# Kernel tuning notes

Hardware: AMD Instinct MI355X
Metric: run time of the kernel (lower is better)

The kernel has to match this reference:

```python
import jax, jax.numpy as jnp
import numpy as np

B, S, D = 4, 8192, 1024
NC = 5
EPS = 1e-5  # nn.LayerNorm default eps


def setup_inputs() -> dict:
    key = jax.random.key(0)
    kx, kid, kg, kb, ks, kw, kbias = jax.random.split(key, 7)
    x = jax.random.normal(kx, (B, S, D), dtype=jnp.float32)
    compartment_ids = jax.random.randint(kid, (B, S), 0, NC)
    # per-compartment LayerNorm affine params (stacked) and scaling
    gamma = 1.0 + 0.1 * jax.random.normal(kg, (NC, D), dtype=jnp.float32)
    beta = 0.1 * jax.random.normal(kb, (NC, D), dtype=jnp.float32)
    scale = 1.0 + 0.1 * jax.random.normal(ks, (NC,), dtype=jnp.float32)
    # compartment_transition_norm: nn.Linear(d_model, d_model)
    W = jax.random.normal(kw, (D, D), dtype=jnp.float32) / np.sqrt(D)
    b = 0.01 * jax.random.normal(kbias, (D,), dtype=jnp.float32)
    return {"x": x, "compartment_ids": compartment_ids, "gamma": gamma,
            "beta": beta, "scale": scale, "W": W, "b": b}


def reference(x, compartment_ids, gamma, beta, scale, W, b):
    # tokens with id >= NC are left untouched (original guard)
    valid = compartment_ids < NC                      # [B,S]
    cid = jnp.clip(compartment_ids, 0, NC - 1)        # safe gather index
    # per-token LayerNorm statistics over last dim (biased variance)
    mu = jnp.mean(x, axis=-1, keepdims=True)
    var = jnp.mean(jnp.square(x - mu), axis=-1, keepdims=True)
    normed = (x - mu) * jax.lax.rsqrt(var + EPS)      # [B,S,D]
    g = gamma[cid]                                    # [B,S,D]
    bt = beta[cid]                                    # [B,S,D]
    s = scale[cid][..., None]                         # [B,S,1]
    y = (normed * g + bt) * s
    y = jnp.where(valid[..., None], y, x)
    # residual transition: x + Linear(x)
    return y + jnp.einsum('bsd,ed->bse', y, W) + b
```

## Files before the change

kernel.cpp:

```cpp
#include <hip/hip_runtime.h>
#include <stdint.h>

#define NCOMP 5
#define DM 1024
#define LN_EPS 1e-5f

typedef __attribute__((ext_vector_type(8))) __bf16 bf16x8;
typedef __attribute__((ext_vector_type(4))) float f32x4;

__device__ __forceinline__ unsigned short f2bf(float f) {
    unsigned u = __builtin_bit_cast(unsigned, f);
    u += 0x7fffu + ((u >> 16) & 1u);
    return (unsigned short)(u >> 16);
}

__global__ __launch_bounds__(256) void ln_w_kernel(
    const float* __restrict__ x, const int* __restrict__ cid,
    const float* __restrict__ gamma, const float* __restrict__ beta,
    const float* __restrict__ scale, const float* __restrict__ W,
    unsigned short* __restrict__ y, unsigned short* __restrict__ Wb, int M)
{
    const int lane = threadIdx.x & 63;
    const int t = blockIdx.x * 4 + (threadIdx.x >> 6);

    if (t < M) {
        const float* xp = x + (size_t)t * DM;
        float4 v[4];
#pragma unroll
        for (int q = 0; q < 4; ++q)
            v[q] = *(const float4*)(xp + q * 256 + lane * 4);

        float s = 0.f, ss = 0.f;
#pragma unroll
        for (int q = 0; q < 4; ++q) {
            s  += v[q].x + v[q].y + v[q].z + v[q].w;
            ss += v[q].x*v[q].x + v[q].y*v[q].y + v[q].z*v[q].z + v[q].w*v[q].w;
        }
#pragma unroll
        for (int off = 32; off; off >>= 1) {
            s  += __shfl_xor(s, off);
            ss += __shfl_xor(ss, off);
        }
        const float mu  = s * (1.0f / DM);
        const float var = ss * (1.0f / DM) - mu * mu;
        const float rs  = rsqrtf(var + LN_EPS);

        const int craw  = cid[t];
        const bool valid = craw < NCOMP;
        const int c = min(max(craw, 0), NCOMP - 1);
        const float sc = scale[c];
        const float* gp = gamma + (size_t)c * DM;
        const float* bp = beta  + (size_t)c * DM;
        unsigned short* yp = y + (size_t)t * DM;
#pragma unroll
        for (int q = 0; q < 4; ++q) {
            const int e = q * 256 + lane * 4;
            const float4 g  = *(const float4*)(gp + e);
            const float4 bb = *(const float4*)(bp + e);
            const float o0 = valid ? ((v[q].x - mu) * rs * g.x + bb.x) * sc : v[q].x;
            const float o1 = valid ? ((v[q].y - mu) * rs * g.y + bb.y) * sc : v[q].y;
            const float o2 = valid ? ((v[q].z - mu) * rs * g.z + bb.z) * sc : v[q].z;
            const float o3 = valid ? ((v[q].w - mu) * rs * g.w + bb.w) * sc : v[q].w;
            uint2 p;
            p.x = (unsigned)f2bf(o0) | ((unsigned)f2bf(o1) << 16);
            p.y = (unsigned)f2bf(o2) | ((unsigned)f2bf(o3) << 16);
            *(uint2*)(yp + e) = p;
        }
    } else if (t < M + DM) {
        const int row = t - M;
        const float* wp = W + (size_t)row * DM;
        unsigned short* wo = Wb + (size_t)row * DM;
#pragma unroll
        for (int q = 0; q < 4; ++q) {
            const int e = q * 256 + lane * 4;
            float4 a = *(const float4*)(wp + e);
            a.x += (e + 0 == row) ? 1.0f : 0.0f;
            a.y += (e + 1 == row) ? 1.0f : 0.0f;
            a.z += (e + 2 == row) ? 1.0f : 0.0f;
            a.w += (e + 3 == row) ? 1.0f : 0.0f;
            uint2 p;
            p.x = (unsigned)f2bf(a.x) | ((unsigned)f2bf(a.y) << 16);
            p.y = (unsigned)f2bf(a.z) | ((unsigned)f2bf(a.w) << 16);
            *(uint2*)(wo + e) = p;
        }
    }
}

__device__ __forceinline__ void gld16(const unsigned short* g, unsigned short* l) {
    __builtin_amdgcn_global_load_lds(
        (const __attribute__((address_space(1))) unsigned int*)(uintptr_t)g,
        (__attribute__((address_space(3))) unsigned int*)(uintptr_t)l,
        16, 0, 0);
}

#define GEMM_ITER(T, CA, CAB, CB, NA, NAB, NB)                                \
  {                                                                           \
    const int t_ = (T);                                                       \
                \
    __builtin_amdgcn_s_setprio(1);                                            \
    _Pragma("unroll")                                                         \
    for (int j = 0; j < 4; ++j)                                               \
        _Pragma("unroll")                                                     \
        for (int n = 0; n < 4; ++n)                                           \
            acc[j][n] = __builtin_amdgcn_mfma_f32_16x16x32_bf16(              \
                CB[n], CA[j], acc[j][n], 0, 0, 0);                            \
    __builtin_amdgcn_s_setprio(0);                                            \
                                 \
    if (t_ < 29) {                                                            \
        unsigned short* stg = smem + ((t_ + 3) & 3) * BUF;                    \
        const int kn = (t_ + 3) * 32;                                         \
        gld16(gA0 + kn, stg + sA0);                                           \
        gld16(gA1 + kn, stg + sA1);                                           \
        gld16(gB0 + kn, stg + sB0);                                           \
        gld16(gB1 + kn, stg + sB1);                                           \
    }                                                                         \
       \
    if (t_ < 29)       { asm volatile("s_waitcnt vmcnt(8)" ::: "memory"); }   \
    else if (t_ == 29) { asm volatile("s_waitcnt vmcnt(4)" ::: "memory"); }   \
    else               { asm volatile("s_waitcnt vmcnt(0)" ::: "memory"); }   \
    __builtin_amdgcn_s_barrier();         \
                \
    if (t_ < 31) {                                                            \
        const unsigned short* An = smem + ((t_ + 1) & 3) * BUF;               \
        const unsigned short* Bn = An + 8192;                                 \
        _Pragma("unroll")                                                     \
        for (int j = 0; j < 4; ++j)                                           \
            NB[j] = *(const bf16x8*)&Bn[(wn + j * 16) * 32 + loff];           \
        _Pragma("unroll")                                                     \
        for (int j = 0; j < 4; ++j)                                           \
            NA[j] = *(const bf16x8*)&An[(wm + j * 16) * 32 + loff];           \
    }                                                                         \
              \
    __builtin_amdgcn_s_setprio(1);                                            \
    _Pragma("unroll")                                                         \
    for (int j = 0; j < 4; ++j)                                               \
        _Pragma("unroll")                                                     \
        for (int n = 0; n < 4; ++n)                                           \
            acc[4 + j][n] = __builtin_amdgcn_mfma_f32_16x16x32_bf16(          \
                CB[n], CAB[j], acc[4 + j][n], 0, 0, 0);                       \
    __builtin_amdgcn_s_setprio(0);                                            \
             \
    if (t_ < 31) {                                                            \
        const unsigned short* An = smem + ((t_ + 1) & 3) * BUF;               \
        _Pragma("unroll")                                                     \
        for (int j = 0; j < 4; ++j)                                           \
            NAB[j] = *(const bf16x8*)&An[(wm + 64 + j * 16) * 32 + loff];     \
    }                                                                         \
  }

__global__ __launch_bounds__(512, 2) void gemm_kernel(
    const unsigned short* __restrict__ A,
    const unsigned short* __restrict__ Bp,
    const float* __restrict__ bias,
    float* __restrict__ C, int M)
{
    constexpr int K = 1024, N = 1024;
    constexpr int BUF = 16384;
    __shared__ __align__(16) unsigned short smem[4 * BUF];

    const int tid  = threadIdx.x;
    const int lane = tid & 63;
    const int wave = tid >> 6;
    const int wm   = (wave >> 2) * 128;
    const int wn   = (wave & 3) * 64;

    const int nwg = gridDim.x;
    int wg = blockIdx.x;
    if ((nwg & 7) == 0) wg = (wg & 7) * (nwg >> 3) + (wg >> 3);
    const int bm = (wg >> 2) * 256;
    const int bn = (wg & 3) * 256;

    const int qsrc = (((lane & 3) ^ ((lane >> 3) & 3))) * 8;
    const int rA0  = (wave * 2) * 16 + (lane >> 2);
    const unsigned short* gA0 = A  + (size_t)(bm + rA0) * K + qsrc;
    const unsigned short* gA1 = A  + (size_t)(bm + rA0 + 16) * K + qsrc;
    const unsigned short* gB0 = Bp + (size_t)(bn + rA0) * K + qsrc;
    const unsigned short* gB1 = Bp + (size_t)(bn + rA0 + 16) * K + qsrc;
    const int sA0 = (wave * 2) * 512 + lane * 8;
    const int sA1 = sA0 + 512;
    const int sB0 = 8192 + sA0;
    const int sB1 = 8192 + sA1;

    const int fr   = lane & 15;
    const int quad = lane >> 4;
    const int loff = fr * 32 + ((quad ^ ((fr >> 1) & 3)) * 8);

    f32x4 acc[8][4] = {};

#pragma unroll
    for (int kt = 0; kt < 3; ++kt) {
        unsigned short* sb = smem + kt * BUF;
        gld16(gA0 + kt * 32, sb + sA0);
        gld16(gA1 + kt * 32, sb + sA1);
        gld16(gB0 + kt * 32, sb + sB0);
        gld16(gB1 + kt * 32, sb + sB1);
    }
    asm volatile("s_waitcnt vmcnt(8)" ::: "memory");
    __builtin_amdgcn_s_barrier();

    bf16x8 afA0[4], afB0[4], bfr0[4], afA1[4], afB1[4], bfr1[4];
    {
        const unsigned short* A0 = smem;
        const unsigned short* B0 = smem + 8192;
#pragma unroll
        for (int j = 0; j < 4; ++j)
            bfr0[j] = *(const bf16x8*)&B0[(wn + j * 16) * 32 + loff];
#pragma unroll
        for (int j = 0; j < 4; ++j)
            afA0[j] = *(const bf16x8*)&A0[(wm + j * 16) * 32 + loff];
#pragma unroll
        for (int j = 0; j < 4; ++j)
            afB0[j] = *(const bf16x8*)&A0[(wm + 64 + j * 16) * 32 + loff];
    }

    for (int t = 0; t < 32; t += 2) {
        GEMM_ITER(t,     afA0, afB0, bfr0, afA1, afB1, bfr1)
        GEMM_ITER(t + 1, afA1, afB1, bfr1, afA0, afB0, bfr0)
    }

    float* tb = (float*)smem + wave * 1088;
    const int q4 = quad * 4;
    const float4 bvT = *(const float4*)&bias[bn + wn + fr * 4];
#pragma unroll
    for (int mi = 0; mi < 8; ++mi) {
#pragma unroll
        for (int ni = 0; ni < 4; ++ni)
            *(float4*)&tb[fr * 68 + ni * 16 + q4] = *(const float4*)&acc[mi][ni];
#pragma unroll
        for (int j = 0; j < 4; ++j) {
            const int row = j * 4 + quad;
            const float4 v = *(const float4*)&tb[row * 68 + fr * 4];
            float4 o;
            o.x = v.x + bvT.x; o.y = v.y + bvT.y;
            o.z = v.z + bvT.z; o.w = v.w + bvT.w;
            *(float4*)&C[(size_t)(bm + wm + mi * 16 + row) * N + bn + wn + fr * 4] = o;
        }
    }
}

extern "C" void kernel_launch(void* const* d_in, const int* in_sizes, int n_in,
                              void* d_out, int out_size, void* d_ws, size_t ws_size,
                              hipStream_t stream)
{
    const float* x     = (const float*)d_in[0];
    const int*   cid   = (const int*)d_in[1];
    const float* gamma = (const float*)d_in[2];
    const float* beta  = (const float*)d_in[3];
    const float* scale = (const float*)d_in[4];
    const float* W     = (const float*)d_in[5];
    const float* bias  = (const float*)d_in[6];
    float* out = (float*)d_out;

    const int M = in_sizes[0] / DM;
    unsigned short* yb = (unsigned short*)d_ws;
    unsigned short* Wb = yb + (size_t)M * DM;

    ln_w_kernel<<<(M + DM) / 4, 256, 0, stream>>>(x, cid, gamma, beta, scale, W, yb, Wb, M);
    gemm_kernel<<<dim3((M / 256) * 4), 512, 0, stream>>>(yb, Wb, bias, out, M);
}
```

Measured before the change: 307.4 us.

## Process two output tiles per GEMM workgroup with cross-tile prefetch

Each GEMM workgroup now computes two 256x256 output tiles in sequence and halves the grid. During the first tile's final k-steps it prefetches the second tile's first stages, so the pipeline does not drain between tiles. The epilogue moves to a swizzled staging buffer in the fourth LDS stage so it does not overwrite prefetched data. This amortises prologue/epilogue latency, but leaves fewer workgroups and may hurt load balance or occupancy.

```diff
diff --git a/kernel.cpp b/kernel.cpp
--- a/kernel.cpp
+++ b/kernel.cpp
@@ -93,7 +93,7 @@
         16, 0, 0);
 }
 
-#define GEMM_ITER(T, CA, CAB, CB, NA, NAB, NB)                                \
+#define GEMM_ITER(T, MODE, CA, CAB, CB, NA, NAB, NB)                          \
   {                                                                           \
     const int t_ = (T);                                                       \
                 \
@@ -105,7 +105,7 @@
             acc[j][n] = __builtin_amdgcn_mfma_f32_16x16x32_bf16(              \
                 CB[n], CA[j], acc[j][n], 0, 0, 0);                            \
     __builtin_amdgcn_s_setprio(0);                                            \
-                                 \
+     \
     if (t_ < 29) {                                                            \
         unsigned short* stg = smem + ((t_ + 3) & 3) * BUF;                    \
         const int kn = (t_ + 3) * 32;                                         \
@@ -113,14 +113,23 @@
         gld16(gA1 + kn, stg + sA1);                                           \
         gld16(gB0 + kn, stg + sB0);                                           \
         gld16(gB1 + kn, stg + sB1);                                           \
-    }                                                                         \
-       \
-    if (t_ < 29)       { asm volatile("s_waitcnt vmcnt(8)" ::: "memory"); }   \
-    else if (t_ == 29) { asm volatile("s_waitcnt vmcnt(4)" ::: "memory"); }   \
-    else               { asm volatile("s_waitcnt vmcnt(0)" ::: "memory"); }   \
+    } else if (MODE == 0) {                                                   \
+               \
+        unsigned short* stg = smem + ((t_ + 3) & 3) * BUF;                    \
+        const int kn2 = (t_ - 29) * 32;                                       \
+        gld16(gA0 + kn2 + dA, stg + sA0);                                     \
+        gld16(gA1 + kn2 + dA, stg + sA1);                                     \
+        gld16(gB0 + kn2 + dB, stg + sB0);                                     \
+        gld16(gB1 + kn2 + dB, stg + sB1);                                     \
+    }                                                                         \
+           \
+    if (MODE == 0 || t_ < 29) { asm volatile("s_waitcnt vmcnt(8)" ::: "memory"); } \
+    else if (t_ == 29)        { asm volatile("s_waitcnt vmcnt(4)" ::: "memory"); } \
+    else                      { asm volatile("s_waitcnt vmcnt(0)" ::: "memory"); } \
     __builtin_amdgcn_s_barrier();         \
-                \
-    if (t_ < 31) {                                                            \
+          \
+          \
+    if (MODE == 0 || t_ < 31) {                                               \
         const unsigned short* An = smem + ((t_ + 1) & 3) * BUF;               \
         const unsigned short* Bn = An + 8192;                                 \
         _Pragma("unroll")                                                     \
@@ -140,11 +149,35 @@
                 CB[n], CAB[j], acc[4 + j][n], 0, 0, 0);                       \
     __builtin_amdgcn_s_setprio(0);                                            \
              \
-    if (t_ < 31) {                                                            \
+    if (MODE == 0 || t_ < 31) {                                               \
         const unsigned short* An = smem + ((t_ + 1) & 3) * BUF;               \
         _Pragma("unroll")                                                     \
         for (int j = 0; j < 4; ++j)                                           \
             NAB[j] = *(const bf16x8*)&An[(wm + 64 + j * 16) * 32 + loff];     \
+    }                                                                         \
+  }
+
+#define EPILOGUE()                                                            \
+  {                                                                           \
+    float* tb = (float*)(smem + 3 * BUF) + wave * 1024;                       \
+    const float4 bvT = *(const float4*)&bias[bn + wn + fr * 4];               \
+    _Pragma("unroll")                                                         \
+    for (int mi = 0; mi < 8; ++mi) {                                          \
+        _Pragma("unroll")                                                     \
+        for (int ni = 0; ni < 4; ++ni)                                        \
+            *(float4*)&tb[fr * 64 + (((ni * 4 + quad) ^ ((fr & 7) << 1)) * 4)]\
+                = *(const float4*)&acc[mi][ni];                               \
+        _Pragma("unroll")                                                     \
+        for (int j = 0; j < 4; ++j) {                                         \
+            const int row = j * 4 + quad;                                     \
+            const float4 v = *(const float4*)                                 \
+                &tb[row * 64 + ((fr ^ ((row & 7) << 1)) * 4)];                \
+            float4 o;                                                         \
+            o.x = v.x + bvT.x; o.y = v.y + bvT.y;                             \
+            o.z = v.z + bvT.z; o.w = v.w + bvT.w;                             \
+            *(float4*)&C[(size_t)(bm + wm + mi * 16 + row) * N                \
+                         + bn + wn + fr * 4] = o;                             \
+        }                                                                     \
     }                                                                         \
   }
 
@@ -164,11 +197,17 @@
     const int wm   = (wave >> 2) * 128;
     const int wn   = (wave & 3) * 64;
 
-    const int nwg = gridDim.x;
-    int wg = blockIdx.x;
-    if ((nwg & 7) == 0) wg = (wg & 7) * (nwg >> 3) + (wg >> 3);
-    const int bm = (wg >> 2) * 256;
-    const int bn = (wg & 3) * 256;
+    const int nwg = gridDim.x * 2;
+    const int wge0 = blockIdx.x;
+    const int wge1 = blockIdx.x + gridDim.x;
+    const int wg0 = (wge0 & 7) * (nwg >> 3) + (wge0 >> 3);
+    const int wg1 = (wge1 & 7) * (nwg >> 3) + (wge1 >> 3);
+    const int bm0 = (wg0 >> 2) * 256, bn0 = (wg0 & 3) * 256;
+    const int bm1 = (wg1 >> 2) * 256, bn1 = (wg1 & 3) * 256;
+    const ptrdiff_t dA = (ptrdiff_t)(bm1 - bm0) * K;
+    const ptrdiff_t dB = (ptrdiff_t)(bn1 - bn0) * K;
+
+    int bm = bm0, bn = bn0;
 
     const int qsrc = (((lane & 3) ^ ((lane >> 3) & 3))) * 8;
     const int rA0  = (wave * 2) * 16 + (lane >> 2);
@@ -185,6 +224,7 @@
     const int quad = lane >> 4;
     const int loff = fr * 32 + ((quad ^ ((fr >> 1) & 3)) * 8);
 
+    const f32x4 fzero = {0.f, 0.f, 0.f, 0.f};
     f32x4 acc[8][4] = {};
 
 #pragma unroll
@@ -214,28 +254,27 @@
     }
 
     for (int t = 0; t < 32; t += 2) {
-        GEMM_ITER(t,     afA0, afB0, bfr0, afA1, afB1, bfr1)
-        GEMM_ITER(t + 1, afA1, afB1, bfr1, afA0, afB0, bfr0)
-    }
-
-    float* tb = (float*)smem + wave * 1088;
-    const int q4 = quad * 4;
-    const float4 bvT = *(const float4*)&bias[bn + wn + fr * 4];
-#pragma unroll
-    for (int mi = 0; mi < 8; ++mi) {
-#pragma unroll
-        for (int ni = 0; ni < 4; ++ni)
-            *(float4*)&tb[fr * 68 + ni * 16 + q4] = *(const float4*)&acc[mi][ni];
-#pragma unroll
-        for (int j = 0; j < 4; ++j) {
-            const int row = j * 4 + quad;
-            const float4 v = *(const float4*)&tb[row * 68 + fr * 4];
-            float4 o;
-            o.x = v.x + bvT.x; o.y = v.y + bvT.y;
-            o.z = v.z + bvT.z; o.w = v.w + bvT.w;
-            *(float4*)&C[(size_t)(bm + wm + mi * 16 + row) * N + bn + wn + fr * 4] = o;
-        }
-    }
+        GEMM_ITER(t,     0, afA0, afB0, bfr0, afA1, afB1, bfr1)
+        GEMM_ITER(t + 1, 0, afA1, afB1, bfr1, afA0, afB0, bfr0)
+    }
+
+    EPILOGUE()
+    __builtin_amdgcn_s_barrier();
+
+    bm = bm1; bn = bn1;
+    gA0 += dA; gA1 += dA; gB0 += dB; gB1 += dB;
+#pragma unroll
+    for (int j = 0; j < 8; ++j)
+#pragma unroll
+        for (int n = 0; n < 4; ++n)
+            acc[j][n] = fzero;
+
+    for (int t = 0; t < 32; t += 2) {
+        GEMM_ITER(t,     1, afA0, afB0, bfr0, afA1, afB1, bfr1)
+        GEMM_ITER(t + 1, 1, afA1, afB1, bfr1, afA0, afB0, bfr0)
+    }
+
+    EPILOGUE()
 }
 
 extern "C" void kernel_launch(void* const* d_in, const int* in_sizes, int n_in,
@@ -256,5 +295,5 @@
     unsigned short* Wb = yb + (size_t)M * DM;
 
     ln_w_kernel<<<(M + DM) / 4, 256, 0, stream>>>(x, cid, gamma, beta, scale, W, yb, Wb, M);
-    gemm_kernel<<<dim3((M / 256) * 4), 512, 0, stream>>>(yb, Wb, bias, out, M);
-}
+    gemm_kernel<<<dim3((M / 256) * 4 / 2), 512, 0, stream>>>(yb, Wb, bias, out, M);
+}
```

New measurement: 312.1 us. About the same (+1.5%).
